# Performance work log

Hardware: AMD Instinct MI355X
Metric: run time of the kernel (lower is better)

Reference implementation:

```python
import jax, jax.numpy as jnp
import numpy as np

B, C, H, W = 8, 192, 256, 256

def setup_inputs() -> dict:
    key = jax.random.key(0)
    k1, k2, k3, k4, k5 = jax.random.split(key, 5)
    x = jax.random.normal(k1, (B, C, H, W), dtype=jnp.float32)
    w1 = jax.random.normal(k2, (C, 1, 1, 1), dtype=jnp.float32) * 0.1
    w3 = jax.random.normal(k3, (C, 1, 3, 3), dtype=jnp.float32) * 0.1
    w5 = jax.random.normal(k4, (C, 1, 5, 5), dtype=jnp.float32) * 0.1
    alpha = jax.random.normal(k5, (4,), dtype=jnp.float32)
    return {"x": x, "w1": w1, "w3": w3, "w5": w5, "alpha": alpha}

def _dwconv(x, w, pad):
    # depthwise conv: feature_group_count == channels, kernel (C,1,k,k)
    return jax.lax.conv_general_dilated(
        x, w, window_strides=(1, 1), padding=[(pad, pad), (pad, pad)],
        dimension_numbers=("NCHW", "OIHW", "NCHW"),
        feature_group_count=x.shape[1])

def reference(x, w1, w3, w5, alpha):
    out1 = _dwconv(x, w1, 0)
    out3 = _dwconv(x, w3, 1)
    out5 = _dwconv(x, w5, 2)
    return alpha[0] * x + alpha[1] * out1 + alpha[2] * out3 + alpha[3] * out5
```

## Files before the change

### kernel.cpp

```cpp
#include <hip/hip_runtime.h>


typedef float f32x2 __attribute__((ext_vector_type(2)));
typedef float f32x4 __attribute__((ext_vector_type(4)));

constexpr int Bn = 8, Cn = 192, Hn = 256, Wn = 256;
constexpr int TR      = 32;
constexpr int LROWS   = TR + 4;
constexpr int LSTRIDE = 264;
constexpr int BANDS   = Hn / TR;
constexpr int NWG     = Bn * Cn * BANDS;
constexpr int CHUNK   = NWG / 8;

__device__ __forceinline__ float uniformf(float v) {
    return __builtin_bit_cast(float,
        __builtin_amdgcn_readfirstlane(__builtin_bit_cast(int, v)));
}

__device__ __forceinline__ void gload16(const float* g, float* l) {
    __builtin_amdgcn_global_load_lds(
        (const __attribute__((address_space(1))) unsigned int*)g,
        (__attribute__((address_space(3))) unsigned int*)l, 16, 0, 0);
}

__global__ __launch_bounds__(256)
void omnishift_kernel(const float* __restrict__ x,
                      const float* __restrict__ w1,
                      const float* __restrict__ w3,
                      const float* __restrict__ w5,
                      const float* __restrict__ alpha,
                      float* __restrict__ out)
{
    __shared__ float lds[LROWS * LSTRIDE];

    const int tid   = threadIdx.x;
    const int wg    = (blockIdx.x & 7) * CHUNK + (blockIdx.x >> 3);
    const int band  = wg % BANDS;
    const int plane = wg / BANDS;
    const int c     = plane % Cn;
    const int r0    = band * TR;

    const float a0 = alpha[0], a1 = alpha[1], a2 = alpha[2], a3 = alpha[3];
    float wf[5][5];
#pragma unroll
    for (int i = 0; i < 5; ++i)
#pragma unroll
        for (int j = 0; j < 5; ++j) {
            float v = a3 * w5[(c * 5 + i) * 5 + j];
            if (i >= 1 && i <= 3 && j >= 1 && j <= 3)
                v += a2 * w3[(c * 3 + (i - 1)) * 3 + (j - 1)];
            if (i == 2 && j == 2)
                v += a1 * w1[c] + a0;
            wf[i][j] = uniformf(v);
        }

    const float* xp = x + (size_t)plane * (Hn * Wn);

    if (tid < LROWS * 4) {
        const int r   = tid >> 2;
        const int q   = tid & 3;
        const int pos = (q < 2) ? (2 + q) : (258 + q);
        lds[r * LSTRIDE + pos] = 0.f;
    }

#pragma unroll
    for (int i = 0; i < 9; ++i) {
        const int idx = tid + i * 256;
        const int row = idx >> 6;
        const int l   = idx & 63;
        const int gr  = r0 - 2 + row;
        float* dst = &lds[row * LSTRIDE + 4];
        if ((unsigned)gr < (unsigned)Hn) {
            gload16(xp + (size_t)gr * Wn + 4 * l, dst);
        } else {
            f32x2 z = {0.f, 0.f};
            f32x2* d = reinterpret_cast<f32x2*>(dst + 4 * l);
            d[0] = z; d[1] = z;
        }
    }
    __syncthreads();

    const int ct     = tid & 63;
    const int rg     = tid >> 6;
    const int oc0    = 4 * ct;
    const int lrbase = rg * 8;

    float* outp = out + (size_t)plane * (Hn * Wn)
                      + (size_t)(r0 + rg * 8) * Wn + oc0;

    auto ldrow = [&](int lr, float w[8]) {
        const f32x2* src = reinterpret_cast<const f32x2*>(
            &lds[lr * LSTRIDE + oc0 + 2]);
#pragma unroll
        for (int h = 0; h < 4; ++h) {
            f32x2 p = src[h];
            w[2 * h] = p.x; w[2 * h + 1] = p.y;
        }
    };

    float win[5][8];
#pragma unroll
    for (int i = 0; i < 4; ++i) ldrow(lrbase + i, win[i]);

#pragma unroll
    for (int k = 0; k < 8; ++k) {
        ldrow(lrbase + 4 + k, win[4]);

        f32x4 o;
#pragma unroll
        for (int j = 0; j < 4; ++j) {
            float acc = 0.f;
#pragma unroll
            for (int i = 0; i < 5; ++i)
#pragma unroll
                for (int d = 0; d < 5; ++d)
                    acc += win[i][j + d] * wf[i][d];
            o[j] = acc;
        }
        *reinterpret_cast<f32x4*>(outp + (size_t)k * Wn) = o;

#pragma unroll
        for (int i = 0; i < 4; ++i)
#pragma unroll
            for (int j = 0; j < 8; ++j) win[i][j] = win[i + 1][j];
    }
}

extern "C" void kernel_launch(void* const* d_in, const int* in_sizes, int n_in,
                              void* d_out, int out_size, void* d_ws, size_t ws_size,
                              hipStream_t stream)
{
    const float* x     = (const float*)d_in[0];
    const float* w1    = (const float*)d_in[1];
    const float* w3    = (const float*)d_in[2];
    const float* w5    = (const float*)d_in[3];
    const float* alpha = (const float*)d_in[4];
    float* out = (float*)d_out;

    omnishift_kernel<<<NWG, 256, 0, stream>>>(x, w1, w3, w5, alpha, out);
}
```

Before: 149.4 us.

## Process two row bands per workgroup with double-buffered LDS staging

Each workgroup now handles two adjacent 32-row bands. Both bands are loaded into two LDS buffers up front, and a partial vmcnt wait lets compute on the first band begin while the second band's loads are still in flight. Out-of-range halo rows issue a dummy load into a spare row so every thread has the same number of outstanding loads. In exchange, LDS use per workgroup doubles, which may reduce occupancy, and the grid is halved.

```diff
diff --git a/kernel.cpp b/kernel.cpp
--- a/kernel.cpp
+++ b/kernel.cpp
@@ -8,8 +8,9 @@
 constexpr int TR      = 32;
 constexpr int LROWS   = TR + 4;
 constexpr int LSTRIDE = 264;
-constexpr int BANDS   = Hn / TR;
-constexpr int NWG     = Bn * Cn * BANDS;
+constexpr int BROWS   = LROWS + 1;
+constexpr int PAIRS   = Hn / (2 * TR);
+constexpr int NWG     = Bn * Cn * PAIRS;
 constexpr int CHUNK   = NWG / 8;
 
 __device__ __forceinline__ float uniformf(float v) {
@@ -31,14 +32,14 @@
                       const float* __restrict__ alpha,
                       float* __restrict__ out)
 {
-    __shared__ float lds[LROWS * LSTRIDE];
+    __shared__ float lds[2][BROWS * LSTRIDE];
 
     const int tid   = threadIdx.x;
     const int wg    = (blockIdx.x & 7) * CHUNK + (blockIdx.x >> 3);
-    const int band  = wg % BANDS;
-    const int plane = wg / BANDS;
+    const int bb    = wg & 3;
+    const int plane = wg >> 2;
     const int c     = plane % Cn;
-    const int r0    = band * TR;
+    const int r0    = bb * 2 * TR;
 
     const float a0 = alpha[0], a1 = alpha[1], a2 = alpha[2], a3 = alpha[3];
     float wf[5][5];
@@ -54,76 +55,91 @@
             wf[i][j] = uniformf(v);
         }
 
-    const float* xp = x + (size_t)plane * (Hn * Wn);
-
-    if (tid < LROWS * 4) {
-        const int r   = tid >> 2;
-        const int q   = tid & 3;
-        const int pos = (q < 2) ? (2 + q) : (258 + q);
-        lds[r * LSTRIDE + pos] = 0.f;
-    }
+    const float* xp = x   + (size_t)plane * (Hn * Wn);
+    float*       op = out + (size_t)plane * (Hn * Wn);
 
 #pragma unroll
-    for (int i = 0; i < 9; ++i) {
-        const int idx = tid + i * 256;
-        const int row = idx >> 6;
-        const int l   = idx & 63;
-        const int gr  = r0 - 2 + row;
-        float* dst = &lds[row * LSTRIDE + 4];
-        if ((unsigned)gr < (unsigned)Hn) {
-            gload16(xp + (size_t)gr * Wn + 4 * l, dst);
-        } else {
-            f32x2 z = {0.f, 0.f};
-            f32x2* d = reinterpret_cast<f32x2*>(dst + 4 * l);
-            d[0] = z; d[1] = z;
+    for (int b = 0; b < 2; ++b)
+        if (tid < LROWS * 4) {
+            const int r   = tid >> 2;
+            const int q   = tid & 3;
+            const int pos = (q < 2) ? (2 + q) : (258 + q);
+            lds[b][r * LSTRIDE + pos] = 0.f;
         }
-    }
-    __syncthreads();
+
+    auto stage = [&](const int b, const int base) {
+#pragma unroll
+        for (int i = 0; i < 9; ++i) {
+            const int idx = tid + i * 256;
+            const int row = idx >> 6;
+            const int l   = idx & 63;
+            const int gr  = base - 2 + row;
+            if ((unsigned)gr < (unsigned)Hn) {
+                gload16(xp + (size_t)gr * Wn + 4 * l,
+                        &lds[b][row * LSTRIDE + 4]);
+            } else {
+                gload16(xp + 4 * l, &lds[b][LROWS * LSTRIDE + 4]);
+                f32x2 z = {0.f, 0.f};
+                f32x2* d = reinterpret_cast<f32x2*>(
+                    &lds[b][row * LSTRIDE + 4 + 4 * l]);
+                d[0] = z; d[1] = z;
+            }
+        }
+    };
 
     const int ct     = tid & 63;
     const int rg     = tid >> 6;
     const int oc0    = 4 * ct;
     const int lrbase = rg * 8;
 
-    float* outp = out + (size_t)plane * (Hn * Wn)
-                      + (size_t)(r0 + rg * 8) * Wn + oc0;
+    auto compute = [&](const int b, const int rt) {
+        const float* buf = lds[b];
+        auto ldrow = [&](int lr, float w[8]) {
+            const f32x2* src = reinterpret_cast<const f32x2*>(
+                &buf[lr * LSTRIDE + oc0 + 2]);
+#pragma unroll
+            for (int h = 0; h < 4; ++h) {
+                f32x2 p = src[h];
+                w[2 * h] = p.x; w[2 * h + 1] = p.y;
+            }
+        };
 
-    auto ldrow = [&](int lr, float w[8]) {
-        const f32x2* src = reinterpret_cast<const f32x2*>(
-            &lds[lr * LSTRIDE + oc0 + 2]);
+        float* outp = op + (size_t)(rt + rg * 8) * Wn + oc0;
+
+        float win[5][8];
 #pragma unroll
-        for (int h = 0; h < 4; ++h) {
-            f32x2 p = src[h];
-            w[2 * h] = p.x; w[2 * h + 1] = p.y;
+        for (int i = 0; i < 4; ++i) ldrow(lrbase + i, win[i]);
+
+#pragma unroll
+        for (int k = 0; k < 8; ++k) {
+            ldrow(lrbase + 4 + k, win[4]);
+
+            f32x4 o;
+#pragma unroll
+            for (int j = 0; j < 4; ++j) {
+                float acc = 0.f;
+#pragma unroll
+                for (int i = 0; i < 5; ++i)
+#pragma unroll
+                    for (int d = 0; d < 5; ++d)
+                        acc += win[i][j + d] * wf[i][d];
+                o[j] = acc;
+            }
+            *reinterpret_cast<f32x4*>(outp + (size_t)k * Wn) = o;
+
+#pragma unroll
+            for (int i = 0; i < 4; ++i)
+#pragma unroll
+                for (int j = 0; j < 8; ++j) win[i][j] = win[i + 1][j];
         }
     };
 
-    float win[5][8];
-#pragma unroll
-    for (int i = 0; i < 4; ++i) ldrow(lrbase + i, win[i]);
-
-#pragma unroll
-    for (int k = 0; k < 8; ++k) {
-        ldrow(lrbase + 4 + k, win[4]);
-
-        f32x4 o;
-#pragma unroll
-        for (int j = 0; j < 4; ++j) {
-            float acc = 0.f;
-#pragma unroll
-            for (int i = 0; i < 5; ++i)
-#pragma unroll
-                for (int d = 0; d < 5; ++d)
-                    acc += win[i][j + d] * wf[i][d];
-            o[j] = acc;
-        }
-        *reinterpret_cast<f32x4*>(outp + (size_t)k * Wn) = o;
-
-#pragma unroll
-        for (int i = 0; i < 4; ++i)
-#pragma unroll
-            for (int j = 0; j < 8; ++j) win[i][j] = win[i + 1][j];
-    }
+    stage(0, r0);
+    stage(1, r0 + TR);
+    asm volatile("s_waitcnt vmcnt(9) lgkmcnt(0)\n\ts_barrier" ::: "memory");
+    compute(0, r0);
+    asm volatile("s_waitcnt vmcnt(8) lgkmcnt(0)\n\ts_barrier" ::: "memory");
+    compute(1, r0 + TR);
 }
 
 extern "C" void kernel_launch(void* const* d_in, const int* in_sizes, int n_in,
```

After: 152.4 us. 1.02x slower.
